# Kernel tuning notes

Measured on AMD Instinct MI355X. Metric: run time of the kernel, lower is better.

The kernel has to match this reference:

```python
import jax, jax.numpy as jnp
import numpy as np
from jax import lax

STRIDE = 1
PAD = 1
KH = KW = 3


def conv2d(x, w, b=None, stride=STRIDE, pad=PAD):
    out = lax.conv_general_dilated(x, w, (stride, stride), [(pad, pad), (pad, pad)],
                                   dimension_numbers=("NCHW", "OIHW", "NCHW"))
    if b is not None:
        out = out + b[None, :, None, None]
    return out


def deform_conv2d(x, offset, mask, weight, stride=STRIDE, pad=PAD):
    """torchvision.ops.deform_conv2d (v2, single group) semantics."""
    B, C, H, W = x.shape
    Co, Ci, Kh, Kw = weight.shape
    K2 = Kh * Kw
    Ho = (H + 2 * pad - Kh) // stride + 1
    Wo = (W + 2 * pad - Kw) // stride + 1

    off = offset.reshape(B, K2, 2, Ho, Wo)  # [...,0]=dy, [...,1]=dx (row-major kernel order)
    ky = (jnp.arange(K2) // Kw).astype(x.dtype)
    kx = (jnp.arange(K2) % Kw).astype(x.dtype)
    hs = (jnp.arange(Ho) * stride - pad).astype(x.dtype)
    ws = (jnp.arange(Wo) * stride - pad).astype(x.dtype)

    # sampling coords [B, K2, Ho, Wo]
    py = off[:, :, 0] + hs[None, None, :, None] + ky[None, :, None, None]
    px = off[:, :, 1] + ws[None, None, None, :] + kx[None, :, None, None]

    y0 = jnp.floor(py)
    x0 = jnp.floor(px)
    wy1 = py - y0
    wx1 = px - x0
    wy0 = 1.0 - wy1
    wx0 = 1.0 - wx1
    y0i = y0.astype(jnp.int32)
    x0i = x0.astype(jnp.int32)

    xf = x.reshape(B, C, H * W)

    def gather(yi, xi):
        valid = (yi >= 0) & (yi < H) & (xi >= 0) & (xi < W)
        lin = jnp.clip(yi, 0, H - 1) * W + jnp.clip(xi, 0, W - 1)  # [B,K2,Ho,Wo]
        linf = lin.reshape(B, 1, -1)
        g = jnp.take_along_axis(xf, jnp.broadcast_to(linf, (B, C, linf.shape[-1])), axis=2)
        g = g.reshape(B, C, K2, Ho, Wo)
        return g * valid[:, None].astype(x.dtype)

    # bilinear combine, modulated by mask; v: [B, C, K2, Ho, Wo]
    v = ((wy0 * wx0)[:, None] * gather(y0i, x0i)
         + (wy0 * wx1)[:, None] * gather(y0i, x0i + 1)
         + (wy1 * wx0)[:, None] * gather(y0i + 1, x0i)
         + (wy1 * wx1)[:, None] * gather(y0i + 1, x0i + 1))
    v = v * mask[:, None]

    return jnp.einsum('bckhw,ock->bohw', v, weight.reshape(Co, Ci, K2))


def setup_inputs() -> dict:
    key = jax.random.key(0)
    ks = jax.random.split(key, 6)
    B, C, H, W = 2, 256, 64, 64
    Co = 256
    fan = C * KH * KW
    return {
        "x": jax.random.normal(ks[0], (B, C, H, W), jnp.float32),
        "residual": jax.random.normal(ks[1], (B, C, H, W), jnp.float32),
        "offset_w": jax.random.normal(ks[2], (2 * KH * KW, C, KH, KW), jnp.float32) * np.sqrt(2.0 / fan),
        "offset_b": jnp.zeros((2 * KH * KW,), jnp.float32),
        "mod_w": jax.random.normal(ks[3], (KH * KW, C, KH, KW), jnp.float32) * np.sqrt(2.0 / fan),
        "mod_b": jnp.zeros((KH * KW,), jnp.float32),
        "reg_w": jax.random.normal(ks[4], (Co, C, KH, KW), jnp.float32) * np.sqrt(2.0 / fan),
    }


def reference(x, residual, offset_w, offset_b, mod_w, mod_b, reg_w):
    offset = conv2d(residual, offset_w, offset_b)
    modulator = 2.0 * jax.nn.sigmoid(conv2d(x, mod_w, mod_b))
    return deform_conv2d(x, offset, modulator, reg_w)
```

## Files before the change

### kernel.cpp

```cpp
#include <hip/hip_runtime.h>
#include <hip/hip_bf16.h>
#include <math.h>

#define BB 2
#define CC 256
#define HH 64
#define WW 64
#define COo 256
#define HWs 4096
#define K2 9
#define CK 2304

typedef __attribute__((ext_vector_type(4))) float floatx4;
typedef __attribute__((ext_vector_type(8))) short shortx8;

#define O_OFF   0
#define O_MASK  147456
#define O_WBF   221184
#define O_WPK   516096
#define O_XT    10027008
#define O_RT    11075584

__device__ __forceinline__ void gll16(const __hip_bfloat16* g, __hip_bfloat16* l) {
    __builtin_amdgcn_global_load_lds(
        (const __attribute__((address_space(1))) unsigned int*)g,
        (__attribute__((address_space(3))) unsigned int*)l, 16, 0, 0);
}

__device__ __forceinline__ short f2bf(float v) {
    __hip_bfloat16 h = __float2bfloat16(v);
    return *reinterpret_cast<short*>(&h);
}

__device__ __forceinline__ float bf2f(short s) {
    unsigned u = ((unsigned)(unsigned short)s) << 16;
    return __builtin_bit_cast(float, u);
}

__global__ __launch_bounds__(256) void prep_kernel(
    const float* __restrict__ x,
    const float* __restrict__ residual,
    const float* __restrict__ reg_w,
    const float* __restrict__ off_w,
    const float* __restrict__ mod_w,
    __hip_bfloat16* __restrict__ xT,
    __hip_bfloat16* __restrict__ resT,
    __hip_bfloat16* __restrict__ Wbf,
    __hip_bfloat16* __restrict__ Wpk)
{
    int blk = blockIdx.x;
    int t = threadIdx.x;
    if (blk < 2048) {
        int sel = blk >> 10;
        int bk  = blk & 1023;
        int oc = bk & 7;
        int y  = (bk >> 3) & 63;
        int b  = bk >> 9;
        int wo = t & 63;
        int cg = t >> 6;
        int c0 = oc * 32 + cg * 8;
        const float* src = (sel ? residual : x)
                           + ((size_t)(b * CC + c0) * HH + y) * WW + wo;
        shortx8 pk;
#pragma unroll
        for (int j = 0; j < 8; ++j) pk[j] = f2bf(src[(size_t)j * HWs]);
        __hip_bfloat16* dst = sel ? resT : xT;
        *(shortx8*)(dst + ((size_t)b * 4096 + y * 64 + wo) * 256 + c0) = pk;
    } else {
        int idx = (blk - 2048) * 256 + t;
        if (idx < CK * COo) {
            int co = idx / CK;
            int r  = idx - co * CK;
            int k  = r >> 8;
            int c  = r & 255;
            Wbf[idx] = __float2bfloat16(reg_w[(size_t)co * CK + c * 9 + k]);
        }
        if (idx < 147456) {
            int g    = idx / 73728;
            int rem  = idx % 73728;
            int kc   = rem / 9216;
            int r2   = rem % 9216;
            int tap  = r2 / 1024;
            int r3   = r2 & 1023;
            int nf   = r3 >> 9;
            int r4   = r3 & 511;
            int lane = r4 >> 3;
            int j    = r4 & 7;
            int c    = kc * 32 + (lane >> 4) * 8 + j;
            int n    = nf * 16 + (lane & 15);
            float v = 0.f;
            if (g == 0) { if (n < 18) v = off_w[((size_t)n * CC + c) * 9 + tap]; }
            else        { if (n < 9)  v = mod_w[((size_t)n * CC + c) * 9 + tap]; }
            Wpk[idx] = __float2bfloat16(v);
        }
    }
}

__global__ __launch_bounds__(512) void convA2_kernel(
    const __hip_bfloat16* __restrict__ xT,
    const __hip_bfloat16* __restrict__ resT,
    const __hip_bfloat16* __restrict__ Wpk,
    const float* __restrict__ off_b,
    const float* __restrict__ mod_b,
    float* __restrict__ off_out,
    float* __restrict__ mask_out)
{
    int blk = blockIdx.x;
    int tile = blk & 127;
    int g = (blk >> 7) & 1;
    int b = blk >> 8;
    int t = threadIdx.x;
    int lane = t & 63;
    int w = t >> 6;
    int ph = w & 1;
    int ks = w >> 1;
    int ln = lane & 15;
    int quad = lane >> 4;

    const __hip_bfloat16* src = (g ? xT : resT) + (size_t)b * 4096 * 256;
    const __hip_bfloat16* wg  = Wpk + (size_t)g * 73728 + (size_t)ks * 2 * 9216;

    int pix = tile * 32 + ph * 16 + ln;
    int ho = pix >> 6, wo = pix & 63;

    floatx4 acc0 = (floatx4){0.f, 0.f, 0.f, 0.f};
    floatx4 acc1 = (floatx4){0.f, 0.f, 0.f, 0.f};

    if (g == 0) {
#pragma unroll
        for (int tap = 0; tap < 9; ++tap) {
            int ky = tap / 3, kx = tap % 3;
            int r  = ho + ky - 1;
            int cx = wo + kx - 1;
            bool v = (r >= 0) && (r < HH) && (cx >= 0) && (cx < WW);
            int hw = v ? (r * WW + cx) : 0;
            const __hip_bfloat16* abase = src + (size_t)hw * 256 + quad * 8 + ks * 64;
            const __hip_bfloat16* wbase = wg + (size_t)tap * 1024 + lane * 8;
#pragma unroll
            for (int kc = 0; kc < 2; ++kc) {
                shortx8 af = *(const shortx8*)(abase + kc * 32);
                if (!v) {
                    shortx8 zf = {0,0,0,0,0,0,0,0};
                    af = zf;
                }
                shortx8 b0 = *(const shortx8*)(wbase + (size_t)kc * 9216);
                shortx8 b1 = *(const shortx8*)(wbase + (size_t)kc * 9216 + 512);
                acc0 = __builtin_amdgcn_mfma_f32_16x16x32_bf16(af, b0, acc0, 0, 0, 0);
                acc1 = __builtin_amdgcn_mfma_f32_16x16x32_bf16(af, b1, acc1, 0, 0, 0);
            }
        }
    } else {
#pragma unroll
        for (int tap = 0; tap < 9; ++tap) {
            int ky = tap / 3, kx = tap % 3;
            int r  = ho + ky - 1;
            int cx = wo + kx - 1;
            bool v = (r >= 0) && (r < HH) && (cx >= 0) && (cx < WW);
            int hw = v ? (r * WW + cx) : 0;
            const __hip_bfloat16* abase = src + (size_t)hw * 256 + quad * 8 + ks * 64;
            const __hip_bfloat16* wbase = wg + (size_t)tap * 1024 + lane * 8;
#pragma unroll
            for (int kc = 0; kc < 2; ++kc) {
                shortx8 af = *(const shortx8*)(abase + kc * 32);
                if (!v) {
                    shortx8 zf = {0,0,0,0,0,0,0,0};
                    af = zf;
                }
                shortx8 b0 = *(const shortx8*)(wbase + (size_t)kc * 9216);
                acc0 = __builtin_amdgcn_mfma_f32_16x16x32_bf16(af, b0, acc0, 0, 0, 0);
            }
        }
    }

    __shared__ float s_red[8][64][8];
    *(floatx4*)&s_red[w][lane][0] = acc0;
    *(floatx4*)&s_red[w][lane][4] = acc1;
    __syncthreads();
    if (w < 2) {
#pragma unroll
        for (int j = 0; j < 4; ++j) {
            acc0[j] = s_red[w][lane][j]     + s_red[w + 2][lane][j]
                    + s_red[w + 4][lane][j] + s_red[w + 6][lane][j];
            acc1[j] = s_red[w][lane][4 + j]     + s_red[w + 2][lane][4 + j]
                    + s_red[w + 4][lane][4 + j] + s_red[w + 6][lane][4 + j];
        }

#pragma unroll
        for (int nf = 0; nf < 2; ++nf) {
            floatx4 a = nf ? acc1 : acc0;
            int n = nf * 16 + ln;
#pragma unroll
            for (int i2 = 0; i2 < 4; ++i2) {
                int p = tile * 32 + w * 16 + quad * 4 + i2;
                if (g == 0) {
                    if (n < 18)
                        off_out[((size_t)b * 18 + n) * HWs + p] = a[i2] + off_b[n];
                } else {
                    if (n < 9) {
                        float z = a[i2] + mod_b[n];
                        mask_out[((size_t)b * 9 + n) * HWs + p] =
                            2.f / (1.f + __expf(-z));
                    }
                }
            }
        }
    }
}

__global__ __launch_bounds__(1024) void gemm_fused_kernel(
    const __hip_bfloat16* __restrict__ xT,
    const float* __restrict__ off,
    const float* __restrict__ mask,
    const __hip_bfloat16* __restrict__ Wbf,
    float* __restrict__ out)
{
    int blk0 = blockIdx.x;
    int mt = ((blk0 & 7) << 5) | (blk0 >> 3);
    int t  = threadIdx.x;
    int lane = t & 63;
    int w    = t >> 6;
    int quad = lane >> 4;
    int ln   = lane & 15;
    int wm = w & 1;
    int wN = w >> 1;

    __shared__ __hip_bfloat16 As[2][32 * 64];
    __shared__ __hip_bfloat16 Bs[2][256 * 64];
    __shared__ int   s_mi[32][K2][4];
    __shared__ float s_mw[32][K2][4];
    __shared__ float s_out[16][16 * 20];

    int b = mt >> 7;
    const __hip_bfloat16* xb = xT + (size_t)b * 4096 * 256;

    int lr8 = lane >> 3;
    int sub = lane & 7;
    int chk = sub ^ lr8;

    const __hip_bfloat16* gB = Wbf + (size_t)(w * 16 + lr8) * CK + chk * 8;

    floatx4 acc[2];
#pragma unroll
    for (int nf = 0; nf < 2; ++nf) acc[nf] = (floatx4){0.f, 0.f, 0.f, 0.f};

#pragma unroll
    for (int h = 0; h < 2; ++h)
        gll16(gB + (size_t)(h * 8) * CK, &Bs[0][w * 1024 + h * 512]);

    for (int u = t; u < 32 * K2; u += 1024) {
        int pl_ = u / K2;
        int k  = u - pl_ * K2;
        int hw = (mt & 127) * 32 + pl_;
        int ho = hw >> 6, wo = hw & 63;
        float dy = off [(((size_t)b * 18 + 2 * k    ) << 12) + hw];
        float dx = off [(((size_t)b * 18 + 2 * k + 1) << 12) + hw];
        float m  = mask[(((size_t)b * 9  + k        ) << 12) + hw];
        float py = (float)(ho - 1 + k / 3) + dy;
        float px = (float)(wo - 1 + k % 3) + dx;
        float y0f = floorf(py), x0f = floorf(px);
        float wy1 = py - y0f, wx1 = px - x0f;
        float wy0 = 1.f - wy1, wx0 = 1.f - wx1;
        int y0 = (int)y0f, x0 = (int)x0f;
#pragma unroll
        for (int j = 0; j < 4; ++j) {
            int yy = y0 + (j >> 1);
            int xx = x0 + (j & 1);
            float wj = ((j == 0) ? wy0 * wx0 :
                        (j == 1) ? wy0 * wx1 :
                        (j == 2) ? wy1 * wx0 : wy1 * wx1) * m;
            bool valid = (yy >= 0) && (yy < HH) && (xx >= 0) && (xx < WW);
            s_mi[pl_][k][j] = valid ? (yy * WW + xx) : 0;
            s_mw[pl_][k][j] = valid ? wj : 0.f;
        }
    }

    int pl  = (t >> 3) & 31;
    int ch8 = t & 7;
    bool gth = (t < 256);
    int aslot = pl * 64 + ((ch8 ^ (pl & 7)) * 8);

    int   mi0, mi1, mi2, mi3;
    float mw0, mw1, mw2, mw3;
    auto meta_load = [&](int k) {
        mi0 = s_mi[pl][k][0]; mi1 = s_mi[pl][k][1];
        mi2 = s_mi[pl][k][2]; mi3 = s_mi[pl][k][3];
        mw0 = s_mw[pl][k][0]; mw1 = s_mw[pl][k][1];
        mw2 = s_mw[pl][k][2]; mw3 = s_mw[pl][k][3];
    };

    shortx8 gc0, gc1, gc2, gc3;
    float   gw0, gw1, gw2, gw3;
    auto gather_load = [&](int cb) {
        const __hip_bfloat16* xr = xb + cb * 64 + ch8 * 8;
        gc0 = *(const shortx8*)(xr + (size_t)mi0 * 256);
        gc1 = *(const shortx8*)(xr + (size_t)mi1 * 256);
        gc2 = *(const shortx8*)(xr + (size_t)mi2 * 256);
        gc3 = *(const shortx8*)(xr + (size_t)mi3 * 256);
        gw0 = mw0; gw1 = mw1; gw2 = mw2; gw3 = mw3;
    };
    auto gather_store = [&](int buf) {
        shortx8 o;
#pragma unroll
        for (int j = 0; j < 8; ++j)
            o[j] = f2bf(gw0 * bf2f(gc0[j]) + gw1 * bf2f(gc1[j])
                      + gw2 * bf2f(gc2[j]) + gw3 * bf2f(gc3[j]));
        *(shortx8*)&As[buf][aslot] = o;
    };

    __syncthreads();
    if (gth) {
        meta_load(0);
        gather_load(0);
        gather_store(0);
        gather_load(1);
    }

    int swz = ln & 7;

    for (int kt = 0; kt < 36; ++kt) {
        int cur = kt & 1;
        int nxt = cur ^ 1;
        __syncthreads();
        if (kt + 1 < 36) {
            int ko = (kt + 1) * 64;
#pragma unroll
            for (int h = 0; h < 2; ++h)
                gll16(gB + (size_t)(h * 8) * CK + ko, &Bs[nxt][w * 1024 + h * 512]);
        }
#pragma unroll
        for (int kh = 0; kh < 2; ++kh) {
            int slot = ((kh * 4 + quad) ^ swz) * 8;
            shortx8 af = *(const shortx8*)
                &As[cur][(wm * 16 + ln) * 64 + slot];
            shortx8 bf[2];
#pragma unroll
            for (int nf = 0; nf < 2; ++nf)
                bf[nf] = *(const shortx8*)
                    &Bs[cur][(wN * 32 + nf * 16 + ln) * 64 + slot];
#pragma unroll
            for (int nf = 0; nf < 2; ++nf)
                acc[nf] = __builtin_amdgcn_mfma_f32_16x16x32_bf16(
                    af, bf[nf], acc[nf], 0, 0, 0);
        }
        if (gth && kt + 1 < 36) gather_store(nxt);
        if (gth && kt + 2 < 36) {
            int k2 = kt + 2;
            if ((k2 & 3) == 0) meta_load(k2 >> 2);
            gather_load(k2 & 3);
        }
    }

    int bb = mt >> 7;
    int hw0 = (mt & 127) * 32 + wm * 16;
    float* sw = &s_out[w][0];
    int co_l = lane >> 2;
    int seg  = lane & 3;
#pragma unroll
    for (int nf = 0; nf < 2; ++nf) {
        *(floatx4*)&sw[ln * 20 + quad * 4] = acc[nf];
        floatx4 v0 = *(const floatx4*)&sw[co_l * 20 + seg * 4];
        int co = wN * 32 + nf * 16 + co_l;
        float* orow = out + ((size_t)(bb * COo + co) << 12) + hw0;
        *(floatx4*)&orow[seg * 4] = v0;
    }
}

extern "C" void kernel_launch(void* const* d_in, const int* in_sizes, int n_in,
                              void* d_out, int out_size, void* d_ws, size_t ws_size,
                              hipStream_t stream)
{
    const float* x     = (const float*)d_in[0];
    const float* resid = (const float*)d_in[1];
    const float* off_w = (const float*)d_in[2];
    const float* off_b = (const float*)d_in[3];
    const float* mod_w = (const float*)d_in[4];
    const float* mod_b = (const float*)d_in[5];
    const float* reg_w = (const float*)d_in[6];
    float* out = (float*)d_out;

    float* ws = (float*)d_ws;
    float* off_buf   = ws + O_OFF;
    float* mask_buf  = ws + O_MASK;
    __hip_bfloat16* Wbf  = (__hip_bfloat16*)(ws + O_WBF);
    __hip_bfloat16* Wpk  = (__hip_bfloat16*)(ws + O_WPK);
    __hip_bfloat16* xT   = (__hip_bfloat16*)(ws + O_XT);
    __hip_bfloat16* resT = (__hip_bfloat16*)(ws + O_RT);

    prep_kernel<<<2048 + (CK * COo + 255) / 256, 256, 0, stream>>>(
        x, resid, reg_w, off_w, mod_w, xT, resT, Wbf, Wpk);

    convA2_kernel<<<512, 512, 0, stream>>>(xT, resT, Wpk, off_b, mod_b,
                                           off_buf, mask_buf);

    gemm_fused_kernel<<<256, 1024, 0, stream>>>(xT, off_buf, mask_buf, Wbf, out);
}
```

Baseline: 129.2 us.

## Fuse offset/mask conv into deformable GEMM kernel via shared memory

```diff
diff --git a/kernel.cpp b/kernel.cpp
--- a/kernel.cpp
+++ b/kernel.cpp
@@ -14,8 +14,6 @@
 typedef __attribute__((ext_vector_type(4))) float floatx4;
 typedef __attribute__((ext_vector_type(8))) short shortx8;
 
-#define O_OFF   0
-#define O_MASK  147456
 #define O_WBF   221184
 #define O_WPK   516096
 #define O_XT    10027008
@@ -96,121 +94,12 @@
     }
 }
 
-__global__ __launch_bounds__(512) void convA2_kernel(
+__global__ __launch_bounds__(1024) void mega_kernel(
     const __hip_bfloat16* __restrict__ xT,
     const __hip_bfloat16* __restrict__ resT,
     const __hip_bfloat16* __restrict__ Wpk,
     const float* __restrict__ off_b,
     const float* __restrict__ mod_b,
-    float* __restrict__ off_out,
-    float* __restrict__ mask_out)
-{
-    int blk = blockIdx.x;
-    int tile = blk & 127;
-    int g = (blk >> 7) & 1;
-    int b = blk >> 8;
-    int t = threadIdx.x;
-    int lane = t & 63;
-    int w = t >> 6;
-    int ph = w & 1;
-    int ks = w >> 1;
-    int ln = lane & 15;
-    int quad = lane >> 4;
-
-    const __hip_bfloat16* src = (g ? xT : resT) + (size_t)b * 4096 * 256;
-    const __hip_bfloat16* wg  = Wpk + (size_t)g * 73728 + (size_t)ks * 2 * 9216;
-
-    int pix = tile * 32 + ph * 16 + ln;
-    int ho = pix >> 6, wo = pix & 63;
-
-    floatx4 acc0 = (floatx4){0.f, 0.f, 0.f, 0.f};
-    floatx4 acc1 = (floatx4){0.f, 0.f, 0.f, 0.f};
-
-    if (g == 0) {
-#pragma unroll
-        for (int tap = 0; tap < 9; ++tap) {
-            int ky = tap / 3, kx = tap % 3;
-            int r  = ho + ky - 1;
-            int cx = wo + kx - 1;
-            bool v = (r >= 0) && (r < HH) && (cx >= 0) && (cx < WW);
-            int hw = v ? (r * WW + cx) : 0;
-            const __hip_bfloat16* abase = src + (size_t)hw * 256 + quad * 8 + ks * 64;
-            const __hip_bfloat16* wbase = wg + (size_t)tap * 1024 + lane * 8;
-#pragma unroll
-            for (int kc = 0; kc < 2; ++kc) {
-                shortx8 af = *(const shortx8*)(abase + kc * 32);
-                if (!v) {
-                    shortx8 zf = {0,0,0,0,0,0,0,0};
-                    af = zf;
-                }
-                shortx8 b0 = *(const shortx8*)(wbase + (size_t)kc * 9216);
-                shortx8 b1 = *(const shortx8*)(wbase + (size_t)kc * 9216 + 512);
-                acc0 = __builtin_amdgcn_mfma_f32_16x16x32_bf16(af, b0, acc0, 0, 0, 0);
-                acc1 = __builtin_amdgcn_mfma_f32_16x16x32_bf16(af, b1, acc1, 0, 0, 0);
-            }
-        }
-    } else {
-#pragma unroll
-        for (int tap = 0; tap < 9; ++tap) {
-            int ky = tap / 3, kx = tap % 3;
-            int r  = ho + ky - 1;
-            int cx = wo + kx - 1;
-            bool v = (r >= 0) && (r < HH) && (cx >= 0) && (cx < WW);
-            int hw = v ? (r * WW + cx) : 0;
-            const __hip_bfloat16* abase = src + (size_t)hw * 256 + quad * 8 + ks * 64;
-            const __hip_bfloat16* wbase = wg + (size_t)tap * 1024 + lane * 8;
-#pragma unroll
-            for (int kc = 0; kc < 2; ++kc) {
-                shortx8 af = *(const shortx8*)(abase + kc * 32);
-                if (!v) {
-                    shortx8 zf = {0,0,0,0,0,0,0,0};
-                    af = zf;
-                }
-                shortx8 b0 = *(const shortx8*)(wbase + (size_t)kc * 9216);
-                acc0 = __builtin_amdgcn_mfma_f32_16x16x32_bf16(af, b0, acc0, 0, 0, 0);
-            }
-        }
-    }
-
-    __shared__ float s_red[8][64][8];
-    *(floatx4*)&s_red[w][lane][0] = acc0;
-    *(floatx4*)&s_red[w][lane][4] = acc1;
-    __syncthreads();
-    if (w < 2) {
-#pragma unroll
-        for (int j = 0; j < 4; ++j) {
-            acc0[j] = s_red[w][lane][j]     + s_red[w + 2][lane][j]
-                    + s_red[w + 4][lane][j] + s_red[w + 6][lane][j];
-            acc1[j] = s_red[w][lane][4 + j]     + s_red[w + 2][lane][4 + j]
-                    + s_red[w + 4][lane][4 + j] + s_red[w + 6][lane][4 + j];
-        }
-
-#pragma unroll
-        for (int nf = 0; nf < 2; ++nf) {
-            floatx4 a = nf ? acc1 : acc0;
-            int n = nf * 16 + ln;
-#pragma unroll
-            for (int i2 = 0; i2 < 4; ++i2) {
-                int p = tile * 32 + w * 16 + quad * 4 + i2;
-                if (g == 0) {
-                    if (n < 18)
-                        off_out[((size_t)b * 18 + n) * HWs + p] = a[i2] + off_b[n];
-                } else {
-                    if (n < 9) {
-                        float z = a[i2] + mod_b[n];
-                        mask_out[((size_t)b * 9 + n) * HWs + p] =
-                            2.f / (1.f + __expf(-z));
-                    }
-                }
-            }
-        }
-    }
-}
-
-__global__ __launch_bounds__(1024) void gemm_fused_kernel(
-    const __hip_bfloat16* __restrict__ xT,
-    const float* __restrict__ off,
-    const float* __restrict__ mask,
     const __hip_bfloat16* __restrict__ Wbf,
     float* __restrict__ out)
 {
@@ -229,6 +118,8 @@
     __shared__ int   s_mi[32][K2][4];
     __shared__ float s_mw[32][K2][4];
     __shared__ float s_out[16][16 * 20];
+    __shared__ float s_off[32][18];
+    __shared__ float s_msk[32][9];
 
     int b = mt >> 7;
     const __hip_bfloat16* xb = xT + (size_t)b * 4096 * 256;
@@ -246,15 +137,123 @@
 #pragma unroll
     for (int h = 0; h < 2; ++h)
         gll16(gB + (size_t)(h * 8) * CK, &Bs[0][w * 1024 + h * 512]);
+
+    {
+        int cg  = w >> 3;
+        int wr  = w & 7;
+        int cph = wr & 1;
+        int cks = wr >> 1;
+        const __hip_bfloat16* csrc = (cg ? xT : resT) + (size_t)b * 4096 * 256;
+        const __hip_bfloat16* cwg  = Wpk + (size_t)cg * 73728
+                                         + (size_t)cks * 2 * 9216;
+        int cpix = (mt & 127) * 32 + cph * 16 + ln;
+        int cho = cpix >> 6, cwo = cpix & 63;
+
+        floatx4 ca0 = (floatx4){0.f, 0.f, 0.f, 0.f};
+        floatx4 ca1 = (floatx4){0.f, 0.f, 0.f, 0.f};
+
+        if (cg == 0) {
+#pragma unroll
+            for (int tap = 0; tap < 9; ++tap) {
+                int ky = tap / 3, kx = tap % 3;
+                int r  = cho + ky - 1;
+                int cx = cwo + kx - 1;
+                bool v = (r >= 0) && (r < HH) && (cx >= 0) && (cx < WW);
+                int hw = v ? (r * WW + cx) : 0;
+                const __hip_bfloat16* abase = csrc + (size_t)hw * 256
+                                              + quad * 8 + cks * 64;
+                const __hip_bfloat16* wbase = cwg + (size_t)tap * 1024 + lane * 8;
+#pragma unroll
+                for (int kc = 0; kc < 2; ++kc) {
+                    shortx8 af = *(const shortx8*)(abase + kc * 32);
+                    if (!v) {
+                        shortx8 zf = {0,0,0,0,0,0,0,0};
+                        af = zf;
+                    }
+                    shortx8 b0 = *(const shortx8*)(wbase + (size_t)kc * 9216);
+                    shortx8 b1 = *(const shortx8*)(wbase + (size_t)kc * 9216 + 512);
+                    ca0 = __builtin_amdgcn_mfma_f32_16x16x32_bf16(af, b0, ca0, 0, 0, 0);
+                    ca1 = __builtin_amdgcn_mfma_f32_16x16x32_bf16(af, b1, ca1, 0, 0, 0);
+                }
+            }
+        } else {
+#pragma unroll
+            for (int tap = 0; tap < 9; ++tap) {
+                int ky = tap / 3, kx = tap % 3;
+                int r  = cho + ky - 1;
+                int cx = cwo + kx - 1;
+                bool v = (r >= 0) && (r < HH) && (cx >= 0) && (cx < WW);
+                int hw = v ? (r * WW + cx) : 0;
+                const __hip_bfloat16* abase = csrc + (size_t)hw * 256
+                                              + quad * 8 + cks * 64;
+                const __hip_bfloat16* wbase = cwg + (size_t)tap * 1024 + lane * 8;
+#pragma unroll
+                for (int kc = 0; kc < 2; ++kc) {
+                    shortx8 af = *(const shortx8*)(abase + kc * 32);
+                    if (!v) {
+                        shortx8 zf = {0,0,0,0,0,0,0,0};
+                        af = zf;
+                    }
+                    shortx8 b0 = *(const shortx8*)(wbase + (size_t)kc * 9216);
+                    ca0 = __builtin_amdgcn_mfma_f32_16x16x32_bf16(af, b0, ca0, 0, 0, 0);
+                }
+            }
+        }
+
+        float* s_red = (float*)&Bs[1][0];
+        *(floatx4*)&s_red[((size_t)w * 64 + lane) * 8]     = ca0;
+        *(floatx4*)&s_red[((size_t)w * 64 + lane) * 8 + 4] = ca1;
+    }
+    __syncthreads();
+
+    {
+        int cg = w >> 3;
+        int wr = w & 7;
+        if (wr < 2) {
+            float* s_red = (float*)&Bs[1][0];
+            floatx4 a0, a1;
+#pragma unroll
+            for (int j = 0; j < 4; ++j) {
+                int base = cg * 8 + wr;
+                a0[j] = s_red[(((size_t)base     * 64 + lane)) * 8 + j]
+                      + s_red[(((size_t)(base+2) * 64 + lane)) * 8 + j]
+                      + s_red[(((size_t)(base+4) * 64 + lane)) * 8 + j]
+                      + s_red[(((size_t)(base+6) * 64 + lane)) * 8 + j];
+                a1[j] = s_red[(((size_t)base     * 64 + lane)) * 8 + 4 + j]
+                      + s_red[(((size_t)(base+2) * 64 + lane)) * 8 + 4 + j]
+                      + s_red[(((size_t)(base+4) * 64 + lane)) * 8 + 4 + j]
+                      + s_red[(((size_t)(base+6) * 64 + lane)) * 8 + 4 + j];
+            }
+#pragma unroll
+            for (int nf = 0; nf < 2; ++nf) {
+                floatx4 a = nf ? a1 : a0;
+                int n = nf * 16 + ln;
+#pragma unroll
+                for (int i2 = 0; i2 < 4; ++i2) {
+                    int p = wr * 16 + quad * 4 + i2;
+                    if (cg == 0) {
+                        if (n < 18)
+                            s_off[p][n] = a[i2] + off_b[n];
+                    } else {
+                        if (n < 9) {
+                            float z = a[i2] + mod_b[n];
+                            s_msk[p][n] = 2.f / (1.f + __expf(-z));
+                        }
+                    }
+                }
+            }
+        }
+    }
+    __syncthreads();
 
     for (int u = t; u < 32 * K2; u += 1024) {
         int pl_ = u / K2;
         int k  = u - pl_ * K2;
         int hw = (mt & 127) * 32 + pl_;
         int ho = hw >> 6, wo = hw & 63;
-        float dy = off [(((size_t)b * 18 + 2 * k    ) << 12) + hw];
-        float dx = off [(((size_t)b * 18 + 2 * k + 1) << 12) + hw];
-        float m  = mask[(((size_t)b * 9  + k        ) << 12) + hw];
+        float dy = s_off[pl_][2 * k];
+        float dx = s_off[pl_][2 * k + 1];
+        float m  = s_msk[pl_][k];
         float py = (float)(ho - 1 + k / 3) + dy;
         float px = (float)(wo - 1 + k % 3) + dx;
         float y0f = floorf(py), x0f = floorf(px);
@@ -379,8 +378,6 @@
     float* out = (float*)d_out;
 
     float* ws = (float*)d_ws;
-    float* off_buf   = ws + O_OFF;
-    float* mask_buf  = ws + O_MASK;
     __hip_bfloat16* Wbf  = (__hip_bfloat16*)(ws + O_WBF);
     __hip_bfloat16* Wpk  = (__hip_bfloat16*)(ws + O_WPK);
     __hip_bfloat16* xT   = (__hip_bfloat16*)(ws + O_XT);
@@ -389,8 +386,5 @@
     prep_kernel<<<2048 + (CK * COo + 255) / 256, 256, 0, stream>>>(
         x, resid, reg_w, off_w, mod_w, xT, resT, Wbf, Wpk);
 
-    convA2_kernel<<<512, 512, 0, stream>>>(xT, resT, Wpk, off_b, mod_b,
-                                           off_buf, mask_buf);
-
-    gemm_fused_kernel<<<256, 1024, 0, stream>>>(xT, off_buf, mask_buf, Wbf, out);
-}
+    mega_kernel<<<256, 1024, 0, stream>>>(xT, resT, Wpk, off_b, mod_b, Wbf, out);
+}
```

Result: no change. 127.2 us (-1.6%).
